# Optimization experiments

Measured on AMD Instinct MI355X. Metric: run time of the kernel, lower is better.

The kernel has to match this reference:

```python
import jax, jax.numpy as jnp
import numpy as np

B, S, D, H = 4, 2048, 256, 8  # batch, seq, d_hidden (= per-head dim), n_heads
ROPE_BASE = 10000.0


def _rope_tables(seq_len, dim, dtype=jnp.float32):
    # standard RoPE: inv_freq over half the dim, half-split rotate
    inv_freq = 1.0 / (ROPE_BASE ** (jnp.arange(0, dim, 2, dtype=jnp.float32) / dim))
    angles = jnp.arange(seq_len, dtype=jnp.float32)[:, None] * inv_freq[None, :]  # [S, D/2]
    return jnp.cos(angles).astype(dtype), jnp.sin(angles).astype(dtype)


def _apply_rope(x, cos, sin):
    # x: [..., S, D]; cos/sin: [S, D/2]
    d2 = x.shape[-1] // 2
    x1, x2 = x[..., :d2], x[..., d2:]
    return jnp.concatenate([x1 * cos - x2 * sin, x1 * sin + x2 * cos], axis=-1)


def setup_inputs() -> dict:
    key = jax.random.key(0)
    ks = jax.random.split(key, 5)
    scale_in = 1.0 / np.sqrt(D)
    scale_out = 1.0 / np.sqrt(H * D)
    return {
        "x": jax.random.normal(ks[0], (B, S, D), jnp.float32),
        "w_qkv": jax.random.normal(ks[1], (3 * H * D, D), jnp.float32) * scale_in,
        "b_qkv": jax.random.normal(ks[2], (3 * H * D,), jnp.float32) * 0.02,
        "w_out": jax.random.normal(ks[3], (D, H * D), jnp.float32) * scale_out,
        "b_out": jax.random.normal(ks[4], (D,), jnp.float32) * 0.02,
    }


def reference(x, w_qkv, b_qkv, w_out, b_out):
    b, s, d = x.shape
    # QKV projection: [b, s, 3*H*D]
    qkv = x @ w_qkv.T + b_qkv
    # einops '(qkv heads hidden)': qkv axis outermost -> [b, s, 3, H, D]
    qkv = qkv.reshape(b, s, 3, H, D)
    qkv = jnp.transpose(qkv, (2, 0, 3, 1, 4))  # [3, b, H, s, D]
    q, k, v = qkv[0], qkv[1], qkv[2]
    cos, sin = _rope_tables(s, D, x.dtype)
    q = _apply_rope(q, cos, sin)
    k = _apply_rope(k, cos, sin)
    # non-causal SDPA, scale = 1/sqrt(D)
    scores = jnp.einsum('bhqd,bhkd->bhqk', q, k) / jnp.sqrt(jnp.asarray(D, x.dtype))
    probs = jax.nn.softmax(scores, axis=-1)
    attn = jnp.einsum('bhqk,bhkd->bhqd', probs, v)  # [b, H, s, D]
    # '... heads seq hidden -> ... seq (heads hidden)'
    attn_concat = jnp.transpose(attn, (0, 2, 1, 3)).reshape(b, s, H * D)
    out = attn_concat @ w_out.T + b_out
    return x + out
```

## Files before the change

### kernel.cpp

```cpp
#include <hip/hip_runtime.h>
#include <hip/hip_bf16.h>
#include <stdint.h>

#define Sq   2048
#define Dq   256
#define Hq   8
#define NQKV 6144
#define HD   2048
#define MTOK 8192

typedef __attribute__((ext_vector_type(8))) short short8;
typedef __attribute__((ext_vector_type(4))) float f32x4;
typedef __attribute__((ext_vector_type(16))) float f32x16;
typedef __attribute__((ext_vector_type(4))) int i32x4;

__device__ __forceinline__ float bf2f(short v) {
  union { float f; unsigned u; } x; x.u = ((unsigned)(unsigned short)v) << 16; return x.f;
}
__device__ __forceinline__ short f2bf(float f) {
  union { float f; unsigned u; } x; x.f = f;
  unsigned r = x.u + 0x7fffu + ((x.u >> 16) & 1u);
  return (short)(r >> 16);
}
__device__ __forceinline__ void gload16(const void* g, void* lds) {
  auto g1 = (const __attribute__((address_space(1))) int*)(uintptr_t)g;
  auto l3 = (__attribute__((address_space(3))) int*)(uintptr_t)lds;
  __builtin_amdgcn_global_load_lds(g1, l3, 16, 0, 0);
}
__device__ __forceinline__ float exp2a(float x) {
  float r; asm("v_exp_f32 %0, %1" : "=v"(r) : "v"(x)); return r;
}
__device__ __forceinline__ unsigned cvtpk(float lo, float hi) {
  unsigned r; asm("v_cvt_pk_bf16_f32 %0, %1, %2" : "=v"(r) : "v"(lo), "v"(hi)); return r;
}
__device__ __forceinline__ void plswap(unsigned &a, unsigned &b) {
  asm volatile("v_permlane32_swap_b32 %0, %1" : "+v"(a), "+v"(b));
}

__global__ __launch_bounds__(256) void k_prep(
    const float* __restrict__ x, const float* __restrict__ wqkv,
    const float* __restrict__ wout,
    short* __restrict__ xb, short* __restrict__ wqb, short* __restrict__ wob,
    float* __restrict__ cost, float* __restrict__ sint)
{
  long i = (long)blockIdx.x * 256 + threadIdx.x;
  const long n_x  = (long)MTOK * Dq;
  const long n_wq = (long)NQKV * Dq;
  const long n_wo = (long)Dq * HD;
  const long n_tab = (long)Sq * 128;
  if (i < n_x) { xb[i] = f2bf(x[i]); return; }
  i -= n_x;
  if (i < n_wq) { wqb[i] = f2bf(wqkv[i]); return; }
  i -= n_wq;
  if (i < n_wo) { wob[i] = f2bf(wout[i]); return; }
  i -= n_wo;
  if (i < n_tab) {
    int s = (int)(i >> 7), j = (int)(i & 127);
    double inv = pow(10000.0, -(double)j / 128.0);
    double a = (double)s * inv;
    cost[i] = (float)cos(a);
    sint[i] = (float)sin(a);
  }
}

template<int EPI>
__global__ __launch_bounds__(256, 2) void k_gemm(
    const short* __restrict__ A, const short* __restrict__ Bt,
    const float* __restrict__ bias, const float* __restrict__ resid,
    void* __restrict__ Cp, int M, int N, int K)
{
  __shared__ short As[128 * 64];
  __shared__ short Bs[128 * 64];
  const int tid = threadIdx.x;
  const int w = tid >> 6, lane = tid & 63;
  const int grp = lane >> 4, l15 = lane & 15;
  const int wr = w >> 1, wc = w & 1;
  const int m0 = blockIdx.y * 128, n0 = blockIdx.x * 128;

  f32x4 acc[4][4];
#pragma unroll
  for (int i = 0; i < 4; i++)
#pragma unroll
    for (int j = 0; j < 4; j++) acc[i][j] = f32x4{0.f, 0.f, 0.f, 0.f};

  for (int kt = 0; kt < K; kt += 64) {
#pragma unroll
    for (int r = 0; r < 4; r++) {
      int G = r * 256 + tid;
      int row = G >> 3, gc = G & 7;
      gload16(A + (size_t)(m0 + row) * K + kt + gc * 8,
              (char*)As + (r * 256 + w * 64) * 16);
      gload16(Bt + (size_t)(n0 + row) * K + kt + gc * 8,
              (char*)Bs + (r * 256 + w * 64) * 16);
    }
    __syncthreads();
#pragma unroll
    for (int kk = 0; kk < 2; kk++) {
      short8 af[4], bf[4];
#pragma unroll
      for (int mi = 0; mi < 4; mi++) {
        int row = wr * 64 + mi * 16 + l15;
        af[mi] = *(const short8*)&As[row * 64 + kk * 32 + grp * 8];
      }
#pragma unroll
      for (int ni = 0; ni < 4; ni++) {
        int row = wc * 64 + ni * 16 + l15;
        bf[ni] = *(const short8*)&Bs[row * 64 + kk * 32 + grp * 8];
      }
#pragma unroll
      for (int mi = 0; mi < 4; mi++)
#pragma unroll
        for (int ni = 0; ni < 4; ni++)
          acc[mi][ni] = __builtin_amdgcn_mfma_f32_16x16x32_bf16(
              af[mi], bf[ni], acc[mi][ni], 0, 0, 0);
    }
    __syncthreads();
  }
#pragma unroll
  for (int mi = 0; mi < 4; mi++) {
#pragma unroll
    for (int ni = 0; ni < 4; ni++) {
      int colb = n0 + wc * 64 + ni * 16 + l15;
      float bv = bias[colb];
#pragma unroll
      for (int j = 0; j < 4; j++) {
        int row = m0 + wr * 64 + mi * 16 + grp * 4 + j;
        float v = acc[mi][ni][j] + bv;
        if (EPI == 0) {
          ((short*)Cp)[(size_t)row * N + colb] = f2bf(v);
        } else {
          size_t o = (size_t)row * N + colb;
          ((float*)Cp)[o] = v + resid[o];
        }
      }
    }
  }
}

__global__ __launch_bounds__(256) void k_rope(
    short* __restrict__ qkv, const float* __restrict__ cost,
    const float* __restrict__ sint)
{
  int id = blockIdx.x * 256 + threadIdx.x;
  int jv = id & 15;
  int h = (id >> 4) & 7;
  int t = id >> 7;
  int s = t & (Sq - 1);
  const float QS = 0.090168441f;
  size_t base = (size_t)t * NQKV + h * 256 + jv * 8;
  short8 q1 = *(const short8*)&qkv[base];
  short8 q2 = *(const short8*)&qkv[base + 128];
  short8 k1 = *(const short8*)&qkv[base + 2048];
  short8 k2 = *(const short8*)&qkv[base + 2048 + 128];
  const float* cp = &cost[(size_t)s * 128 + jv * 8];
  const float* sp = &sint[(size_t)s * 128 + jv * 8];
  short8 oq1, oq2, ok1, ok2;
#pragma unroll
  for (int e = 0; e < 8; e++) {
    float c = cp[e], sn = sp[e];
    float a = bf2f(q1[e]), b2 = bf2f(q2[e]);
    oq1[e] = f2bf((a * c - b2 * sn) * QS);
    oq2[e] = f2bf((a * sn + b2 * c) * QS);
    float ka = bf2f(k1[e]), kb = bf2f(k2[e]);
    ok1[e] = f2bf(ka * c - kb * sn);
    ok2[e] = f2bf(ka * sn + kb * c);
  }
  *(short8*)&qkv[base] = oq1;
  *(short8*)&qkv[base + 128] = oq2;
  *(short8*)&qkv[base + 2048] = ok1;
  *(short8*)&qkv[base + 2048 + 128] = ok2;
}

__global__ __launch_bounds__(256) void k_vt(
    const short* __restrict__ qkv, short* __restrict__ vT)
{
  __shared__ short t[64][72];
  int kt = blockIdx.x, dt = blockIdx.y, bh = blockIdx.z;
  int b = bh >> 3, h = bh & 7;
  int tid = threadIdx.x;
  int r = tid >> 2, c0 = (tid & 3) * 16;
  const short* src = &qkv[(size_t)(b * Sq + kt * 64 + r) * NQKV + 4096 + h * 256 + dt * 64 + c0];
  short8 v0 = *(const short8*)src;
  short8 v1 = *(const short8*)(src + 8);
#pragma unroll
  for (int e = 0; e < 8; e++) { t[r][c0 + e] = v0[e]; t[r][c0 + 8 + e] = v1[e]; }
  __syncthreads();
  short8 o0, o1;
#pragma unroll
  for (int e = 0; e < 8; e++) { o0[e] = t[c0 + e][r]; o1[e] = t[c0 + 8 + e][r]; }
  short* dst = &vT[(size_t)(bh * 256 + dt * 64 + r) * Sq + kt * 64 + c0];
  *(short8*)dst = o0;
  *(short8*)(dst + 8) = o1;
}

__global__ __launch_bounds__(256, 2) void k_attn(
    const short* __restrict__ qkv, const short* __restrict__ vT,
    short* __restrict__ attn)
{
  __shared__ short Ks[2][32 * 256];
  __shared__ short Vs[2][256 * 36];
  const int tid = threadIdx.x;
  const int w = tid >> 6, lane = tid & 63;
  const int l31 = lane & 31, hi = lane >> 5;
  const int id = blockIdx.x;
  const int bh = (id & 7) * 4 + ((id >> 3) & 3);
  const int qb0 = (id >> 5) * 128;
  const int b = bh >> 3, h = bh & 7;

  short8 qf[16];
  {
    const short* qbase = &qkv[(size_t)(b * Sq + qb0 + w * 32 + l31) * NQKV + h * 256 + hi * 8];
#pragma unroll
    for (int kc = 0; kc < 16; kc++) qf[kc] = *(const short8*)&qbase[kc * 16];
  }
  f32x16 o[8];
#pragma unroll
  for (int dt = 0; dt < 8; dt++)
#pragma unroll
    for (int e = 0; e < 16; e++) o[dt][e] = 0.f;
  float m = -3e38f, l = 0.f;

  const size_t krow0 = (size_t)(b * Sq) * NQKV + 2048 + h * 256;
  const short* vbase = &vT[(size_t)bh * 256 * Sq];

#pragma unroll
  for (int r = 0; r < 4; r++) {
    int G = r * 256 + tid;
    int row = G >> 5, gc = G & 31;
    gload16(&qkv[krow0 + (size_t)row * NQKV + ((gc ^ (row & 7)) * 8)],
            (char*)&Ks[0][0] + (r * 256 + w * 64) * 16);
  }
  {
    short8 v0[4];
#pragma unroll
    for (int r = 0; r < 4; r++) {
      int G = r * 256 + tid;
      v0[r] = *(const short8*)&vbase[(size_t)(G >> 2) * Sq + (G & 3) * 8];
    }
#pragma unroll
    for (int r = 0; r < 4; r++) {
      int G = r * 256 + tid;
      *(short8*)&Vs[0][(G >> 2) * 36 + (G & 3) * 8] = v0[r];
    }
  }
  __syncthreads();

  int cur = 0;
  for (int kt = 0; kt < Sq / 32; kt++) {
    short8 vnext[4];
    if (kt + 1 < Sq / 32) {
#pragma unroll
      for (int r = 0; r < 4; r++) {
        int G = r * 256 + tid;
        int row = G >> 5, gc = G & 31;
        gload16(&qkv[krow0 + (size_t)((kt + 1) * 32 + row) * NQKV + ((gc ^ (row & 7)) * 8)],
                (char*)&Ks[cur ^ 1][0] + (r * 256 + w * 64) * 16);
      }
#pragma unroll
      for (int r = 0; r < 4; r++) {
        int G = r * 256 + tid;
        vnext[r] = *(const short8*)&vbase[(size_t)(G >> 2) * Sq + (kt + 1) * 32 + (G & 3) * 8];
      }
    }

    f32x16 sc;
#pragma unroll
    for (int e = 0; e < 16; e++) sc[e] = 0.f;
    __builtin_amdgcn_s_setprio(1);
#pragma unroll
    for (int kc = 0; kc < 16; kc++) {
      int byteoff = l31 * 512 + (((kc * 2 + hi) ^ (l31 & 7)) << 4);
      short8 ka = *(const short8*)((const char*)&Ks[cur][0] + byteoff);
      sc = __builtin_amdgcn_mfma_f32_32x32x16_bf16(ka, qf[kc], sc, 0, 0, 0);
    }
    __builtin_amdgcn_s_setprio(0);

    float pmax = sc[0];
#pragma unroll
    for (int e = 1; e < 16; e++) pmax = fmaxf(pmax, sc[e]);
    pmax = fmaxf(pmax, __shfl_xor(pmax, 32, 64));
    if (!__all(pmax <= m + 8.0f)) {
      float nm = fmaxf(m, pmax);
      float f = exp2a(m - nm);
      l *= f;
#pragma unroll
      for (int dt = 0; dt < 8; dt++)
#pragma unroll
        for (int e = 0; e < 16; e++) o[dt][e] *= f;
      m = nm;
    }
    float rs = 0.f;
#pragma unroll
    for (int e = 0; e < 16; e++) {
      float p = exp2a(sc[e] - m);
      sc[e] = p;
      rs += p;
    }
    rs += __shfl_xor(rs, 32, 64);
    l += rs;

    short8 pa[2];
    {
      unsigned x0 = cvtpk(sc[0], sc[1]);
      unsigned y0 = cvtpk(sc[4], sc[5]);
      unsigned x1 = cvtpk(sc[2], sc[3]);
      unsigned y1 = cvtpk(sc[6], sc[7]);
      plswap(x0, y0);
      plswap(x1, y1);
      i32x4 w0; w0[0] = x0; w0[1] = x1; w0[2] = y0; w0[3] = y1;
      pa[0] = __builtin_bit_cast(short8, w0);
      unsigned x2 = cvtpk(sc[8],  sc[9]);
      unsigned y2 = cvtpk(sc[12], sc[13]);
      unsigned x3 = cvtpk(sc[10], sc[11]);
      unsigned y3 = cvtpk(sc[14], sc[15]);
      plswap(x2, y2);
      plswap(x3, y3);
      i32x4 w1; w1[0] = x2; w1[1] = x3; w1[2] = y2; w1[3] = y3;
      pa[1] = __builtin_bit_cast(short8, w1);
    }

    __builtin_amdgcn_s_setprio(1);
#pragma unroll
    for (int dt = 0; dt < 8; dt++) {
#pragma unroll
      for (int ks = 0; ks < 2; ks++) {
        short8 vb = *(const short8*)&Vs[cur][(dt * 32 + l31) * 36 + ks * 16 + hi * 8];
        o[dt] = __builtin_amdgcn_mfma_f32_32x32x16_bf16(pa[ks], vb, o[dt], 0, 0, 0);
      }
    }
    __builtin_amdgcn_s_setprio(0);

    if (kt + 1 < Sq / 32) {
#pragma unroll
      for (int r = 0; r < 4; r++) {
        int G = r * 256 + tid;
        *(short8*)&Vs[cur ^ 1][(G >> 2) * 36 + (G & 3) * 8] = vnext[r];
      }
    }
    __syncthreads();
    cur ^= 1;
  }

  float linv = 1.0f / l;
  float li[16];
#pragma unroll
  for (int e = 0; e < 16; e++)
    li[e] = __shfl(linv, (e & 3) + 8 * (e >> 2) + 4 * hi, 64);
  short* orow = &attn[(size_t)(b * Sq + qb0 + w * 32) * HD + h * 256 + l31];
#pragma unroll
  for (int dt = 0; dt < 8; dt++)
#pragma unroll
    for (int e = 0; e < 16; e++)
      orow[(size_t)((e & 3) + 8 * (e >> 2) + 4 * hi) * HD + dt * 32] = f2bf(o[dt][e] * li[e]);
}

extern "C" void kernel_launch(void* const* d_in, const int* in_sizes, int n_in,
                              void* d_out, int out_size, void* d_ws, size_t ws_size,
                              hipStream_t stream) {
  const float* x     = (const float*)d_in[0];
  const float* w_qkv = (const float*)d_in[1];
  const float* b_qkv = (const float*)d_in[2];
  const float* w_out = (const float*)d_in[3];
  const float* b_out = (const float*)d_in[4];
  float* out = (float*)d_out;

  char* ws = (char*)d_ws;
  short* qkv  = (short*)ws;
  short* vT   = (short*)(ws + 100663296);
  short* attn = (short*)(ws + 134217728);
  short* xb   = (short*)(ws + 167772160);
  short* wqb  = (short*)(ws + 171966464);
  short* wob  = (short*)(ws + 175112192);
  float* cost = (float*)(ws + 176160768);
  float* sint = (float*)(ws + 177209344);

  k_prep<<<dim3(17408), 256, 0, stream>>>(x, w_qkv, w_out, xb, wqb, wob, cost, sint);
  k_gemm<0><<<dim3(NQKV / 128, MTOK / 128), 256, 0, stream>>>(
      xb, wqb, b_qkv, nullptr, qkv, MTOK, NQKV, Dq);
  k_rope<<<dim3(4096), 256, 0, stream>>>(qkv, cost, sint);
  k_vt<<<dim3(32, 4, 32), 256, 0, stream>>>(qkv, vT);
  k_attn<<<dim3(512), 256, 0, stream>>>(qkv, vT, attn);
  k_gemm<1><<<dim3(Dq / 128, MTOK / 128), 256, 0, stream>>>(
      attn, wob, b_out, x, out, MTOK, Dq, HD);
}
```

Measured before the change: 372.5 us.

## Use narrower tiles for output GEMM, split QK accumulators, tree reductions, float RoPE tables

The output projection GEMM (N=256) now uses 128x64 tiles, giving twice as many blocks (256 instead of 128) to fill the GPU. Inside the attention kernel, the QK^T MFMA chain alternates between two accumulators to shorten the dependency chain, and the row max and sum use pairwise tree reductions instead of serial ones. The RoPE table generation switches from double-precision pow/sin/cos to float intrinsics, which may slightly change accuracy for large angles.

```diff
diff --git a/kernel.cpp b/kernel.cpp
--- a/kernel.cpp
+++ b/kernel.cpp
@@ -35,6 +35,12 @@
 }
 __device__ __forceinline__ void plswap(unsigned &a, unsigned &b) {
   asm volatile("v_permlane32_swap_b32 %0, %1" : "+v"(a), "+v"(b));
+}
+__device__ __forceinline__ f32x16 fz16() {
+  f32x16 z;
+#pragma unroll
+  for (int e = 0; e < 16; e++) z[e] = 0.f;
+  return z;
 }
 
 __global__ __launch_bounds__(256) void k_prep(
@@ -56,30 +62,34 @@
   i -= n_wo;
   if (i < n_tab) {
     int s = (int)(i >> 7), j = (int)(i & 127);
-    double inv = pow(10000.0, -(double)j / 128.0);
-    double a = (double)s * inv;
-    cost[i] = (float)cos(a);
-    sint[i] = (float)sin(a);
-  }
-}
-
-template<int EPI>
+    float inv = __expf(-(float)j * (9.2103403720f / 128.0f));
+    float a = (float)s * inv;
+    cost[i] = cosf(a);
+    sint[i] = sinf(a);
+  }
+}
+
+template<int EPI, int BN>
 __global__ __launch_bounds__(256, 2) void k_gemm(
     const short* __restrict__ A, const short* __restrict__ Bt,
     const float* __restrict__ bias, const float* __restrict__ resid,
     void* __restrict__ Cp, int M, int N, int K)
 {
+  constexpr int MI = (BN == 128) ? 4 : 2;
+  constexpr int WRS = MI * 16;
+  constexpr int BROUNDS = BN / 32;
   __shared__ short As[128 * 64];
-  __shared__ short Bs[128 * 64];
+  __shared__ short Bs[BN * 64];
   const int tid = threadIdx.x;
   const int w = tid >> 6, lane = tid & 63;
   const int grp = lane >> 4, l15 = lane & 15;
-  const int wr = w >> 1, wc = w & 1;
-  const int m0 = blockIdx.y * 128, n0 = blockIdx.x * 128;
-
-  f32x4 acc[4][4];
-#pragma unroll
-  for (int i = 0; i < 4; i++)
+  const int wr = (BN == 128) ? (w >> 1) : w;
+  const int wc = (BN == 128) ? (w & 1) : 0;
+  const int m0 = blockIdx.y * 128, n0 = blockIdx.x * BN;
+
+  f32x4 acc[MI][4];
+#pragma unroll
+  for (int i = 0; i < MI; i++)
 #pragma unroll
     for (int j = 0; j < 4; j++) acc[i][j] = f32x4{0.f, 0.f, 0.f, 0.f};
 
@@ -90,16 +100,21 @@
       int row = G >> 3, gc = G & 7;
       gload16(A + (size_t)(m0 + row) * K + kt + gc * 8,
               (char*)As + (r * 256 + w * 64) * 16);
+    }
+#pragma unroll
+    for (int r = 0; r < BROUNDS; r++) {
+      int G = r * 256 + tid;
+      int row = G >> 3, gc = G & 7;
       gload16(Bt + (size_t)(n0 + row) * K + kt + gc * 8,
               (char*)Bs + (r * 256 + w * 64) * 16);
     }
     __syncthreads();
 #pragma unroll
     for (int kk = 0; kk < 2; kk++) {
-      short8 af[4], bf[4];
-#pragma unroll
-      for (int mi = 0; mi < 4; mi++) {
-        int row = wr * 64 + mi * 16 + l15;
+      short8 af[MI], bf[4];
+#pragma unroll
+      for (int mi = 0; mi < MI; mi++) {
+        int row = wr * WRS + mi * 16 + l15;
         af[mi] = *(const short8*)&As[row * 64 + kk * 32 + grp * 8];
       }
 #pragma unroll
@@ -108,7 +123,7 @@
         bf[ni] = *(const short8*)&Bs[row * 64 + kk * 32 + grp * 8];
       }
 #pragma unroll
-      for (int mi = 0; mi < 4; mi++)
+      for (int mi = 0; mi < MI; mi++)
 #pragma unroll
         for (int ni = 0; ni < 4; ni++)
           acc[mi][ni] = __builtin_amdgcn_mfma_f32_16x16x32_bf16(
@@ -117,14 +132,14 @@
     __syncthreads();
   }
 #pragma unroll
-  for (int mi = 0; mi < 4; mi++) {
+  for (int mi = 0; mi < MI; mi++) {
 #pragma unroll
     for (int ni = 0; ni < 4; ni++) {
       int colb = n0 + wc * 64 + ni * 16 + l15;
       float bv = bias[colb];
 #pragma unroll
       for (int j = 0; j < 4; j++) {
-        int row = m0 + wr * 64 + mi * 16 + grp * 4 + j;
+        int row = m0 + wr * WRS + mi * 16 + grp * 4 + j;
         float v = acc[mi][ni][j] + bv;
         if (EPI == 0) {
           ((short*)Cp)[(size_t)row * N + colb] = f2bf(v);
@@ -215,9 +230,7 @@
   }
   f32x16 o[8];
 #pragma unroll
-  for (int dt = 0; dt < 8; dt++)
-#pragma unroll
-    for (int e = 0; e < 16; e++) o[dt][e] = 0.f;
+  for (int dt = 0; dt < 8; dt++) o[dt] = fz16();
   float m = -3e38f, l = 0.f;
 
   const size_t krow0 = (size_t)(b * Sq) * NQKV + 2048 + h * 256;
@@ -263,21 +276,27 @@
       }
     }
 
-    f32x16 sc;
-#pragma unroll
-    for (int e = 0; e < 16; e++) sc[e] = 0.f;
+    f32x16 s0 = fz16(), s1 = fz16();
     __builtin_amdgcn_s_setprio(1);
-#pragma unroll
-    for (int kc = 0; kc < 16; kc++) {
-      int byteoff = l31 * 512 + (((kc * 2 + hi) ^ (l31 & 7)) << 4);
-      short8 ka = *(const short8*)((const char*)&Ks[cur][0] + byteoff);
-      sc = __builtin_amdgcn_mfma_f32_32x32x16_bf16(ka, qf[kc], sc, 0, 0, 0);
-    }
+#define QKSTEP(KC, SACC) { \
+      int byteoff = l31 * 512 + ((((KC) * 2 + hi) ^ (l31 & 7)) << 4); \
+      short8 ka = *(const short8*)((const char*)&Ks[cur][0] + byteoff); \
+      SACC = __builtin_amdgcn_mfma_f32_32x32x16_bf16(ka, qf[KC], SACC, 0, 0, 0); }
+    QKSTEP(0, s0)  QKSTEP(1, s1)  QKSTEP(2, s0)  QKSTEP(3, s1)
+    QKSTEP(4, s0)  QKSTEP(5, s1)  QKSTEP(6, s0)  QKSTEP(7, s1)
+    QKSTEP(8, s0)  QKSTEP(9, s1)  QKSTEP(10, s0) QKSTEP(11, s1)
+    QKSTEP(12, s0) QKSTEP(13, s1) QKSTEP(14, s0) QKSTEP(15, s1)
+#undef QKSTEP
     __builtin_amdgcn_s_setprio(0);
-
-    float pmax = sc[0];
-#pragma unroll
-    for (int e = 1; e < 16; e++) pmax = fmaxf(pmax, sc[e]);
+    f32x16 sc = s0 + s1;
+
+    float t8[8];
+#pragma unroll
+    for (int e = 0; e < 8; e++) t8[e] = fmaxf(sc[e], sc[e + 8]);
+#pragma unroll
+    for (int e = 0; e < 4; e++) t8[e] = fmaxf(t8[e], t8[e + 4]);
+    t8[0] = fmaxf(t8[0], t8[2]); t8[1] = fmaxf(t8[1], t8[3]);
+    float pmax = fmaxf(t8[0], t8[1]);
     pmax = fmaxf(pmax, __shfl_xor(pmax, 32, 64));
     if (!__all(pmax <= m + 8.0f)) {
       float nm = fmaxf(m, pmax);
@@ -289,13 +308,15 @@
         for (int e = 0; e < 16; e++) o[dt][e] *= f;
       m = nm;
     }
-    float rs = 0.f;
-#pragma unroll
-    for (int e = 0; e < 16; e++) {
-      float p = exp2a(sc[e] - m);
-      sc[e] = p;
-      rs += p;
-    }
+#pragma unroll
+    for (int e = 0; e < 16; e++) sc[e] = exp2a(sc[e] - m);
+    float r8[8];
+#pragma unroll
+    for (int e = 0; e < 8; e++) r8[e] = sc[e] + sc[e + 8];
+#pragma unroll
+    for (int e = 0; e < 4; e++) r8[e] = r8[e] + r8[e + 4];
+    r8[0] += r8[2]; r8[1] += r8[3];
+    float rs = r8[0] + r8[1];
     rs += __shfl_xor(rs, 32, 64);
     l += rs;
 
@@ -375,11 +396,11 @@
   float* sint = (float*)(ws + 177209344);
 
   k_prep<<<dim3(17408), 256, 0, stream>>>(x, w_qkv, w_out, xb, wqb, wob, cost, sint);
-  k_gemm<0><<<dim3(NQKV / 128, MTOK / 128), 256, 0, stream>>>(
+  k_gemm<0, 128><<<dim3(NQKV / 128, MTOK / 128), 256, 0, stream>>>(
       xb, wqb, b_qkv, nullptr, qkv, MTOK, NQKV, Dq);
   k_rope<<<dim3(4096), 256, 0, stream>>>(qkv, cost, sint);
   k_vt<<<dim3(32, 4, 32), 256, 0, stream>>>(qkv, vT);
   k_attn<<<dim3(512), 256, 0, stream>>>(qkv, vT, attn);
-  k_gemm<1><<<dim3(Dq / 128, MTOK / 128), 256, 0, stream>>>(
+  k_gemm<1, 64><<<dim3(Dq / 64, MTOK / 128), 256, 0, stream>>>(
       attn, wob, b_out, x, out, MTOK, Dq, HD);
 }
```

Measured after the change: 385.8 us. 1.04x slower.
